# Kernel optimization log

Measured on AMD Instinct MI355X. Metric: run time of the kernel, lower is better.

## Reference

```python
import jax, jax.numpy as jnp
import numpy as np

N = 100000      # nodes
DEG = 16        # fixed degree
E = N * DEG     # edges
C_IN = 128
C_OUT = 128


def setup_inputs() -> dict:
    key = jax.random.key(0)
    k1, k2, k3, k4, k5 = jax.random.split(key, 5)
    x = jax.random.normal(k1, (N, C_IN), dtype=jnp.float32)
    # glorot-ish init for the dense weight
    scale = jnp.sqrt(6.0 / (C_IN + C_OUT)).astype(jnp.float32)
    weight = jax.random.uniform(k2, (C_IN, C_OUT), dtype=jnp.float32, minval=-1.0, maxval=1.0) * scale
    bias = jax.random.normal(k3, (C_OUT,), dtype=jnp.float32) * 0.02
    # fixed-degree CSR: every node has DEG in-edges; CSC analogously
    rowptr = (jnp.arange(N + 1, dtype=jnp.int32) * DEG)
    colind = jax.random.randint(k4, (E,), 0, N, dtype=jnp.int32)
    colptr = (jnp.arange(N + 1, dtype=jnp.int32) * DEG)
    rowind = jax.random.randint(k5, (E,), 0, N, dtype=jnp.int32)
    return {"x": x, "weight": weight, "bias": bias,
            "rowptr": rowptr, "colind": colind,
            "colptr": colptr, "rowind": rowind}


def _deg_inv_sqrt(indptr, dtype):
    deg = (indptr[1:] - indptr[:-1]).astype(dtype)
    return (1.0 / jnp.sqrt(deg))[:, None]  # [N, 1]


def reference(x, weight, bias, rowptr, colind, colptr, rowind):
    # dense transform: [N, C_in] @ [C_in, C_out]
    h = x @ weight
    in_norm = _deg_inv_sqrt(rowptr, h.dtype)    # 1/sqrt(in-degree)
    out_norm = _deg_inv_sqrt(colptr, h.dtype)   # 1/sqrt(out-degree)
    h = h * out_norm
    # CSR SpMM (unweighted): out[i] = sum_{e in [rowptr[i], rowptr[i+1])} h[colind[e]]
    n_nodes = rowptr.shape[0] - 1
    n_edges = colind.shape[0]
    row = jnp.searchsorted(rowptr, jnp.arange(n_edges, dtype=rowptr.dtype), side="right") - 1
    aggr = jax.ops.segment_sum(h[colind], row, num_segments=n_nodes)
    aggr = aggr * in_norm + bias
    return aggr
```

## Files before the change

### kernel.cpp

```cpp
#include <hip/hip_runtime.h>
#include <hip/hip_bf16.h>

#define N_NODES 100000
#define DEG 16
#define C 128
#define NTILES 6250
#define GEMM_BLOCKS 256
#define GEMM_WAVES 8

typedef __attribute__((ext_vector_type(8))) short short8;
typedef __attribute__((ext_vector_type(4))) float f32x4;

__device__ inline unsigned short f2bf(float f) {
    unsigned int u = __builtin_bit_cast(unsigned int, f);
    u += 0x7fffu + ((u >> 16) & 1u);
    return (unsigned short)(u >> 16);
}
__device__ inline float bflo(unsigned int p) { return __builtin_bit_cast(float, p << 16); }
__device__ inline float bfhi(unsigned int p) { return __builtin_bit_cast(float, p & 0xffff0000u); }

__global__ __launch_bounds__(512, 2)
void gcn_gemm_kernel(const float* __restrict__ x, const float* __restrict__ w,
                     const int* __restrict__ colptr, unsigned short* __restrict__ h)
{
    __shared__ unsigned short wfrag[32 * 64 * 8];

    int tid = threadIdx.x;
    for (int i = tid; i < C * C; i += 512) {
        int k = i >> 7, n = i & 127;
        int nt = n >> 4, lr = n & 15;
        int kc = k >> 5, quad = (k >> 3) & 3, j = k & 7;
        wfrag[((((nt << 2) + kc) << 6) + (quad << 4) + lr) * 8 + j] = f2bf(w[i]);
    }
    __syncthreads();

    int wave = tid >> 6;
    int lane = tid & 63;
    int lrow = lane & 15;
    int quad = lane >> 4;

    short8 bf[8][4];
#pragma unroll
    for (int nt = 0; nt < 8; ++nt)
#pragma unroll
        for (int kc = 0; kc < 4; ++kc)
            bf[nt][kc] = *reinterpret_cast<const short8*>(
                &wfrag[((((nt << 2) + kc) << 6) + lane) * 8]);

    int tile = blockIdx.x * GEMM_WAVES + wave;
    if (tile >= NTILES) return;
    const int tstride = GEMM_BLOCKS * GEMM_WAVES;

    f32x4 xb[8];
    {
        const float* xr = x + (long)(tile * 16 + lrow) * C + quad * 8;
#pragma unroll
        for (int kc = 0; kc < 4; ++kc) {
            xb[2*kc]   = *reinterpret_cast<const f32x4*>(xr + kc * 32);
            xb[2*kc+1] = *reinterpret_cast<const f32x4*>(xr + kc * 32 + 4);
        }
    }

    while (true) {
        int m0 = tile * 16;
        short8 af[4];
#pragma unroll
        for (int kc = 0; kc < 4; ++kc) {
            short8 a;
            a[0] = (short)f2bf(xb[2*kc][0]);   a[1] = (short)f2bf(xb[2*kc][1]);
            a[2] = (short)f2bf(xb[2*kc][2]);   a[3] = (short)f2bf(xb[2*kc][3]);
            a[4] = (short)f2bf(xb[2*kc+1][0]); a[5] = (short)f2bf(xb[2*kc+1][1]);
            a[6] = (short)f2bf(xb[2*kc+1][2]); a[7] = (short)f2bf(xb[2*kc+1][3]);
            af[kc] = a;
        }
        float onorm[4];
#pragma unroll
        for (int r = 0; r < 4; ++r) {
            int gm = m0 + quad * 4 + r;
            onorm[r] = rsqrtf((float)(colptr[gm + 1] - colptr[gm]));
        }

        int next = tile + tstride;
        bool more = next < NTILES;
        if (more) {
            const float* xr = x + (long)(next * 16 + lrow) * C + quad * 8;
#pragma unroll
            for (int kc = 0; kc < 4; ++kc) {
                xb[2*kc]   = *reinterpret_cast<const f32x4*>(xr + kc * 32);
                xb[2*kc+1] = *reinterpret_cast<const f32x4*>(xr + kc * 32 + 4);
            }
        }

#pragma unroll
        for (int nt = 0; nt < 8; ++nt) {
            f32x4 acc = {0.f, 0.f, 0.f, 0.f};
#pragma unroll
            for (int kc = 0; kc < 4; ++kc)
                acc = __builtin_amdgcn_mfma_f32_16x16x32_bf16(af[kc], bf[nt][kc], acc, 0, 0, 0);
            unsigned short* hp = h + (long)(m0 + quad * 4) * C + nt * 16 + lrow;
#pragma unroll
            for (int r = 0; r < 4; ++r)
                hp[r * C] = f2bf(acc[r] * onorm[r]);
        }
        if (!more) break;
        tile = next;
    }
}

__global__ __launch_bounds__(256, 6)
void gcn_aggr_kernel(const unsigned short* __restrict__ h,
                     const int* __restrict__ rowptr,
                     const int* __restrict__ colind,
                     const float* __restrict__ bias,
                     float* __restrict__ out)
{
    int tid = threadIdx.x;
    int wave = tid >> 6;
    int lane = tid & 63;
    int node0 = (blockIdx.x * 4 + wave) * 2;
    int node1 = node0 + 1;

    int cg = lane & 15;
    int eg = lane >> 4;

    int base0 = rowptr[node0];
    int deg0  = rowptr[node0 + 1] - base0;
    int base1 = rowptr[node1];
    int deg1  = rowptr[node1 + 1] - base1;
    float innorm0 = rsqrtf((float)deg0);
    float innorm1 = rsqrtf((float)deg1);

    int myidx0 = colind[base0 + cg];
    int myidx1 = colind[base1 + cg];

    int4 v0[4], v1[4];
#pragma unroll
    for (int it = 0; it < 4; ++it) {
        int e = it * 4 + eg;
        int j0 = __shfl(myidx0, e);
        int j1 = __shfl(myidx1, e);
        v0[it] = *reinterpret_cast<const int4*>(h + (long)j0 * C + cg * 8);
        v1[it] = *reinterpret_cast<const int4*>(h + (long)j1 * C + cg * 8);
    }

    float acc0[8], acc1[8];
#pragma unroll
    for (int i = 0; i < 8; ++i) { acc0[i] = 0.f; acc1[i] = 0.f; }

#pragma unroll
    for (int it = 0; it < 4; ++it) {
        unsigned int p;
        p = (unsigned int)v0[it].x; acc0[0] += bflo(p); acc0[1] += bfhi(p);
        p = (unsigned int)v0[it].y; acc0[2] += bflo(p); acc0[3] += bfhi(p);
        p = (unsigned int)v0[it].z; acc0[4] += bflo(p); acc0[5] += bfhi(p);
        p = (unsigned int)v0[it].w; acc0[6] += bflo(p); acc0[7] += bfhi(p);
        p = (unsigned int)v1[it].x; acc1[0] += bflo(p); acc1[1] += bfhi(p);
        p = (unsigned int)v1[it].y; acc1[2] += bflo(p); acc1[3] += bfhi(p);
        p = (unsigned int)v1[it].z; acc1[4] += bflo(p); acc1[5] += bfhi(p);
        p = (unsigned int)v1[it].w; acc1[6] += bflo(p); acc1[7] += bfhi(p);
    }

#pragma unroll
    for (int i = 0; i < 8; ++i) {
        acc0[i] += __shfl_xor(acc0[i], 16);
        acc0[i] += __shfl_xor(acc0[i], 32);
        acc1[i] += __shfl_xor(acc1[i], 16);
        acc1[i] += __shfl_xor(acc1[i], 32);
    }

    if (eg < 2) {
        float inn = (eg == 0) ? innorm0 : innorm1;
        int   nd  = (eg == 0) ? node0 : node1;
        float* a  = (eg == 0) ? acc0 : acc1;
        const f32x4* bp = reinterpret_cast<const f32x4*>(bias + cg * 8);
        f32x4 b0 = bp[0], b1 = bp[1];
        f32x4 o0, o1;
        o0[0] = a[0] * inn + b0[0];
        o0[1] = a[1] * inn + b0[1];
        o0[2] = a[2] * inn + b0[2];
        o0[3] = a[3] * inn + b0[3];
        o1[0] = a[4] * inn + b1[0];
        o1[1] = a[5] * inn + b1[1];
        o1[2] = a[6] * inn + b1[2];
        o1[3] = a[7] * inn + b1[3];
        float* op = out + (long)nd * C + cg * 8;
        *reinterpret_cast<f32x4*>(op)     = o0;
        *reinterpret_cast<f32x4*>(op + 4) = o1;
    }
}

extern "C" void kernel_launch(void* const* d_in, const int* in_sizes, int n_in,
                              void* d_out, int out_size, void* d_ws, size_t ws_size,
                              hipStream_t stream) {
    const float* x      = (const float*)d_in[0];
    const float* w      = (const float*)d_in[1];
    const float* bias   = (const float*)d_in[2];
    const int*   rowptr = (const int*)d_in[3];
    const int*   colind = (const int*)d_in[4];
    const int*   colptr = (const int*)d_in[5];
    float* out = (float*)d_out;
    unsigned short* h = (unsigned short*)d_ws;

    gcn_gemm_kernel<<<GEMM_BLOCKS, 512, 0, stream>>>(x, w, colptr, h);
    gcn_aggr_kernel<<<12500, 256, 0, stream>>>(h, rowptr, colind, bias, out);
}
```

Measured before the change: 174.6 us.

## Remap aggregation so each 16-lane group owns one node and loops all edges

The aggregation kernel now gives each 16-lane group of a wave its own node, four nodes per wave instead of two. Each lane gathers all 16 neighbour rows for its 8-channel slice, so the cross-lane shuffle reduction and the idle half of lanes at the output store both go away. Every lane now writes output and the grid is halved. In exchange each thread holds 16 int4 loads in flight, which raises register pressure, so the launch-bounds occupancy hint drops from 6 to 4.

Result: no change. 176.9 us (+1.3%).

```diff
diff --git a/kernel.cpp b/kernel.cpp
--- a/kernel.cpp
+++ b/kernel.cpp
@@ -107,7 +107,7 @@
     }
 }
 
-__global__ __launch_bounds__(256, 6)
+__global__ __launch_bounds__(256, 4)
 void gcn_aggr_kernel(const unsigned short* __restrict__ h,
                      const int* __restrict__ rowptr,
                      const int* __restrict__ colind,
@@ -117,76 +117,52 @@
     int tid = threadIdx.x;
     int wave = tid >> 6;
     int lane = tid & 63;
-    int node0 = (blockIdx.x * 4 + wave) * 2;
-    int node1 = node0 + 1;
+    int g  = lane >> 4;
+    int cl = lane & 15;
 
-    int cg = lane & 15;
-    int eg = lane >> 4;
+    int node = (blockIdx.x * 4 + wave) * 4 + g;
 
-    int base0 = rowptr[node0];
-    int deg0  = rowptr[node0 + 1] - base0;
-    int base1 = rowptr[node1];
-    int deg1  = rowptr[node1 + 1] - base1;
-    float innorm0 = rsqrtf((float)deg0);
-    float innorm1 = rsqrtf((float)deg1);
+    int base = rowptr[node];
+    int deg  = rowptr[node + 1] - base;
+    float innorm = rsqrtf((float)deg);
 
-    int myidx0 = colind[base0 + cg];
-    int myidx1 = colind[base1 + cg];
+    int myidx = colind[base + cl];
 
-    int4 v0[4], v1[4];
+    const unsigned short* hc = h + cl * 8;
+    int4 v[16];
 #pragma unroll
-    for (int it = 0; it < 4; ++it) {
-        int e = it * 4 + eg;
-        int j0 = __shfl(myidx0, e);
-        int j1 = __shfl(myidx1, e);
-        v0[it] = *reinterpret_cast<const int4*>(h + (long)j0 * C + cg * 8);
-        v1[it] = *reinterpret_cast<const int4*>(h + (long)j1 * C + cg * 8);
+    for (int e = 0; e < 16; ++e) {
+        int j = __shfl(myidx, (lane & 48) + e);
+        v[e] = *reinterpret_cast<const int4*>(hc + (long)j * C);
     }
 
-    float acc0[8], acc1[8];
+    float acc[8];
 #pragma unroll
-    for (int i = 0; i < 8; ++i) { acc0[i] = 0.f; acc1[i] = 0.f; }
+    for (int i = 0; i < 8; ++i) acc[i] = 0.f;
 
 #pragma unroll
-    for (int it = 0; it < 4; ++it) {
+    for (int e = 0; e < 16; ++e) {
         unsigned int p;
-        p = (unsigned int)v0[it].x; acc0[0] += bflo(p); acc0[1] += bfhi(p);
-        p = (unsigned int)v0[it].y; acc0[2] += bflo(p); acc0[3] += bfhi(p);
-        p = (unsigned int)v0[it].z; acc0[4] += bflo(p); acc0[5] += bfhi(p);
-        p = (unsigned int)v0[it].w; acc0[6] += bflo(p); acc0[7] += bfhi(p);
-        p = (unsigned int)v1[it].x; acc1[0] += bflo(p); acc1[1] += bfhi(p);
-        p = (unsigned int)v1[it].y; acc1[2] += bflo(p); acc1[3] += bfhi(p);
-        p = (unsigned int)v1[it].z; acc1[4] += bflo(p); acc1[5] += bfhi(p);
-        p = (unsigned int)v1[it].w; acc1[6] += bflo(p); acc1[7] += bfhi(p);
+        p = (unsigned int)v[e].x; acc[0] += bflo(p); acc[1] += bfhi(p);
+        p = (unsigned int)v[e].y; acc[2] += bflo(p); acc[3] += bfhi(p);
+        p = (unsigned int)v[e].z; acc[4] += bflo(p); acc[5] += bfhi(p);
+        p = (unsigned int)v[e].w; acc[6] += bflo(p); acc[7] += bfhi(p);
     }
 
-#pragma unroll
-    for (int i = 0; i < 8; ++i) {
-        acc0[i] += __shfl_xor(acc0[i], 16);
-        acc0[i] += __shfl_xor(acc0[i], 32);
-        acc1[i] += __shfl_xor(acc1[i], 16);
-        acc1[i] += __shfl_xor(acc1[i], 32);
-    }
-
-    if (eg < 2) {
-        float inn = (eg == 0) ? innorm0 : innorm1;
-        int   nd  = (eg == 0) ? node0 : node1;
-        float* a  = (eg == 0) ? acc0 : acc1;
-        const f32x4* bp = reinterpret_cast<const f32x4*>(bias + cg * 8);
-        f32x4 b0 = bp[0], b1 = bp[1];
-        f32x4 o0, o1;
-        o0[0] = a[0] * inn + b0[0];
-        o0[1] = a[1] * inn + b0[1];
-        o0[2] = a[2] * inn + b0[2];
-        o0[3] = a[3] * inn + b0[3];
-        o1[0] = a[4] * inn + b1[0];
-        o1[1] = a[5] * inn + b1[1];
-        o1[2] = a[6] * inn + b1[2];
-        o1[3] = a[7] * inn + b1[3];
-        float* op = out + (long)nd * C + cg * 8;
-        *reinterpret_cast<f32x4*>(op)     = o0;
-        *reinterpret_cast<f32x4*>(op + 4) = o1;
-    }
+    const f32x4* bp = reinterpret_cast<const f32x4*>(bias + cl * 8);
+    f32x4 b0 = bp[0], b1 = bp[1];
+    f32x4 o0, o1;
+    o0[0] = acc[0] * innorm + b0[0];
+    o0[1] = acc[1] * innorm + b0[1];
+    o0[2] = acc[2] * innorm + b0[2];
+    o0[3] = acc[3] * innorm + b0[3];
+    o1[0] = acc[4] * innorm + b1[0];
+    o1[1] = acc[5] * innorm + b1[1];
+    o1[2] = acc[6] * innorm + b1[2];
+    o1[3] = acc[7] * innorm + b1[3];
+    float* op = out + (long)node * C + cl * 8;
+    *reinterpret_cast<f32x4*>(op)     = o0;
+    *reinterpret_cast<f32x4*>(op + 4) = o1;
 }
 
 extern "C" void kernel_launch(void* const* d_in, const int* in_sizes, int n_in,
@@ -202,5 +178,5 @@
     unsigned short* h = (unsigned short*)d_ws;
 
     gcn_gemm_kernel<<<GEMM_BLOCKS, 512, 0, stream>>>(x, w, colptr, h);
-    gcn_aggr_kernel<<<12500, 256, 0, stream>>>(h, rowptr, colind, bias, out);
+    gcn_aggr_kernel<<<6250, 256, 0, stream>>>(h, rowptr, colind, bias, out);
 }
```
